# Optimization experiments

Measured on AMD Instinct MI355X. Metric: run time of the kernel, lower is better.

The kernel has to match this reference:

```python
import jax, jax.numpy as jnp
import numpy as np

B, T, C = 32, 256, 512
MAX_LEN = 25


def setup_inputs() -> dict:
    key = jax.random.key(0)
    ks = jax.random.split(key, 6)
    scale = 1.0 / np.sqrt(C)
    return {
        "word_features": jax.random.normal(ks[0], (B, T, C), dtype=jnp.float32),
        "word_fc_w": jax.random.normal(ks[1], (C, C), dtype=jnp.float32) * scale,
        "word_fc_b": jax.random.normal(ks[2], (C,), dtype=jnp.float32) * scale,
        "pos_emb": jax.random.normal(ks[3], (MAX_LEN, C), dtype=jnp.float32),
        "atten_w": jax.random.normal(ks[4], (C,), dtype=jnp.float32) * scale,
        "atten_b": jax.random.normal(ks[5], (1,), dtype=jnp.float32) * scale,
    }


def reference(word_features, word_fc_w, word_fc_b, pos_emb, atten_w, atten_b):
    # word_fc: (b,t,c) -> (b,t,c)
    wf = jnp.einsum("btc,dc->btd", word_features, word_fc_w) + word_fc_b
    # additive (Bahdanau) attention scores over t for each of max_len query positions
    # add_features: (b, L, t, c) = wf[:,None,:,:] + pos_emb[None,:,None,:]
    add_features = jnp.tanh(wf[:, None, :, :] + pos_emb[None, :, None, :])
    # atten_fc: (b, L, t, 1) -> squeeze -> (b, L, t)
    scores = jnp.einsum("bltc,c->blt", add_features, atten_w) + atten_b[0]
    attn = jax.nn.softmax(scores, axis=2)  # softmax over t
    # bmm: (b,L,t) @ (b,t,c) -> (b,L,c)
    pvam_features = jnp.einsum("blt,btc->blc", attn, wf)
    return pvam_features
```

## Files before the change

kernel.cpp:

```cpp
#include <hip/hip_runtime.h>

#define Bn 32
#define Tn 256
#define Cn 512
#define Ln 25

typedef _Float16 h8 __attribute__((ext_vector_type(8)));
typedef _Float16 h8v __attribute__((ext_vector_type(8)));
typedef __attribute__((ext_vector_type(4))) float f32x4;

#define SCALE2LOG2E 2.885390081777927f

#if __has_builtin(__builtin_amdgcn_exp2f)
#define EXP2(x) __builtin_amdgcn_exp2f(x)
#else
#define EXP2(x) __expf(0.69314718056f * (x))
#endif

#define DPP_ADD(v, ctrl) \
    ((v) + __int_as_float(__builtin_amdgcn_update_dpp(0, __float_as_int(v), ctrl, 0xf, 0xf, true)))

#define NA_OCT (Bn * Tn * Cn / 8)
#define NW_OCT (Cn * Cn / 8)
__global__ __launch_bounds__(256) void k_convert(
        const float* __restrict__ A, const float* __restrict__ W,
        _Float16* __restrict__ A2, _Float16* __restrict__ W2) {
    int idx = blockIdx.x * 256 + threadIdx.x;
    const float* src;
    _Float16* dst;
    int off;
    if (idx < NA_OCT) { src = A; dst = A2; off = idx * 8; }
    else              { src = W; dst = W2; off = (idx - NA_OCT) * 8; }
    float4 v0 = *(const float4*)&src[off];
    float4 v1 = *(const float4*)&src[off + 4];
    h8v o;
    o[0] = (_Float16)v0.x; o[1] = (_Float16)v0.y;
    o[2] = (_Float16)v0.z; o[3] = (_Float16)v0.w;
    o[4] = (_Float16)v1.x; o[5] = (_Float16)v1.y;
    o[6] = (_Float16)v1.z; o[7] = (_Float16)v1.w;
    *(h8v*)&dst[off] = o;
}

#define BM 128
#define BN 64
#define BKg 64
__global__ __launch_bounds__(256) void k_gemm(
        const _Float16* __restrict__ A2, const _Float16* __restrict__ W2,
        const float* __restrict__ bias, float* __restrict__ wf) {
    __shared__ _Float16 As[BM * BKg];
    __shared__ _Float16 Ws[BN * BKg];
    const int tid  = threadIdx.x;
    const int lane = tid & 63;
    const int wv   = tid >> 6;
    const int m0 = blockIdx.y * BM;
    const int n0 = blockIdx.x * BN;
    const int wm = (wv >> 1) * 64;
    const int wn = (wv & 1) * 32;
    const int r = lane & 15, q = lane >> 4;

    const _Float16* gA[4];
    const _Float16* gW[2];
    #pragma unroll
    for (int rr = 0; rr < 4; ++rr) {
        int p = rr * 256 + tid;
        int row = p >> 3, pk = p & 7;
        int lk = pk ^ (row & 7);
        gA[rr] = A2 + (size_t)(m0 + row) * Cn + lk * 8;
    }
    #pragma unroll
    for (int rr = 0; rr < 2; ++rr) {
        int p = rr * 256 + tid;
        int row = p >> 3, pk = p & 7;
        int lk = pk ^ (row & 7);
        gW[rr] = W2 + (size_t)(n0 + row) * Cn + lk * 8;
    }

    f32x4 acc[4][2];
    #pragma unroll
    for (int mi = 0; mi < 4; ++mi)
        #pragma unroll
        for (int ni = 0; ni < 2; ++ni) acc[mi][ni] = (f32x4){0.f, 0.f, 0.f, 0.f};

    for (int kt = 0; kt < Cn / BKg; ++kt) {
        __syncthreads();
        #pragma unroll
        for (int rr = 0; rr < 4; ++rr) {
            __builtin_amdgcn_global_load_lds(
                (const __attribute__((address_space(1))) unsigned int*)gA[rr],
                (__attribute__((address_space(3))) unsigned int*)(As + (rr * 256 + wv * 64) * 8),
                16, 0, 0);
            gA[rr] += BKg;
        }
        #pragma unroll
        for (int rr = 0; rr < 2; ++rr) {
            __builtin_amdgcn_global_load_lds(
                (const __attribute__((address_space(1))) unsigned int*)gW[rr],
                (__attribute__((address_space(3))) unsigned int*)(Ws + (rr * 256 + wv * 64) * 8),
                16, 0, 0);
            gW[rr] += BKg;
        }
        __syncthreads();

        h8 af[4][2], bfr[2][2];
        #pragma unroll
        for (int mi = 0; mi < 4; ++mi)
            #pragma unroll
            for (int kk = 0; kk < 2; ++kk) {
                int row = wm + mi * 16 + r;
                int phys = (kk * 4 + q) ^ (r & 7);
                af[mi][kk] = *(const h8*)&As[row * BKg + phys * 8];
            }
        #pragma unroll
        for (int ni = 0; ni < 2; ++ni)
            #pragma unroll
            for (int kk = 0; kk < 2; ++kk) {
                int row = wn + ni * 16 + r;
                int phys = (kk * 4 + q) ^ (r & 7);
                bfr[ni][kk] = *(const h8*)&Ws[row * BKg + phys * 8];
            }
        #pragma unroll
        for (int kk = 0; kk < 2; ++kk)
            #pragma unroll
            for (int mi = 0; mi < 4; ++mi)
                #pragma unroll
                for (int ni = 0; ni < 2; ++ni)
                    acc[mi][ni] = __builtin_amdgcn_mfma_f32_16x16x32_f16(
                        af[mi][kk], bfr[ni][kk], acc[mi][ni], 0, 0, 0);
    }

    #pragma unroll
    for (int ni = 0; ni < 2; ++ni) {
        const float bv = bias[n0 + wn + ni * 16 + r];
        #pragma unroll
        for (int mi = 0; mi < 4; ++mi)
            #pragma unroll
            for (int reg = 0; reg < 4; ++reg) {
                int row = m0 + wm + mi * 16 + q * 4 + reg;
                int col = n0 + wn + ni * 16 + r;
                wf[(size_t)row * Cn + col] = acc[mi][ni][reg] + bv;
            }
    }
}

__global__ __launch_bounds__(512) void k_scores(
        const float* __restrict__ wf, const float* __restrict__ pos,
        const float* __restrict__ aw, float* __restrict__ scores) {
    __shared__ float part[4 * Ln * 8];
    const int tid  = threadIdx.x;
    const int lane = tid & 63;
    const int wv   = tid >> 6;
    const int tl   = wv >> 1;
    const int ch   = wv & 1;
    const int t    = blockIdx.x * 4 + tl;
    const int b    = blockIdx.y;
    const int co   = ch * 256 + lane * 4;

    float4 w = *(const float4*)&wf[(b * Tn + t) * Cn + co];
    w.x *= SCALE2LOG2E; w.y *= SCALE2LOG2E; w.z *= SCALE2LOG2E; w.w *= SCALE2LOG2E;
    const float4 a = *(const float4*)&aw[co];
    const float U = (a.x + a.y) + (a.z + a.w);
    float4 u;
    u.x = -2.f * a.x; u.y = -2.f * a.y; u.z = -2.f * a.z; u.w = -2.f * a.w;

    const float* pp = pos + co;
    float* prt = &part[tl * Ln * 8 + ch * 4 + (lane >> 4)];
    const bool writer = ((lane & 15) == 0);

    #pragma unroll
    for (int lo = 0; lo < 5; ++lo) {
        float4 pv[5];
        #pragma unroll
        for (int j = 0; j < 5; ++j)
            pv[j] = *(const float4*)(pp + (lo * 5 + j) * Cn);
        #pragma unroll
        for (int j = 0; j < 5; ++j) {
            const float4 p = pv[j];
            float s = U;
            s = fmaf(u.x, __builtin_amdgcn_rcpf(1.f + EXP2(fmaf(SCALE2LOG2E, p.x, w.x))), s);
            s = fmaf(u.y, __builtin_amdgcn_rcpf(1.f + EXP2(fmaf(SCALE2LOG2E, p.y, w.y))), s);
            s = fmaf(u.z, __builtin_amdgcn_rcpf(1.f + EXP2(fmaf(SCALE2LOG2E, p.z, w.z))), s);
            s = fmaf(u.w, __builtin_amdgcn_rcpf(1.f + EXP2(fmaf(SCALE2LOG2E, p.w, w.w))), s);
            s = DPP_ADD(s, 0xB1);
            s = DPP_ADD(s, 0x4E);
            s = DPP_ADD(s, 0x141);
            s = DPP_ADD(s, 0x140);
            if (writer) prt[(lo * 5 + j) * 8] = s;
        }
    }
    __syncthreads();
    if (tid < 4 * Ln) {
        int tl2 = tid / Ln, l2 = tid - tl2 * Ln;
        const float* q = &part[(tl2 * Ln + l2) * 8];
        float v = ((q[0] + q[1]) + (q[2] + q[3])) + ((q[4] + q[5]) + (q[6] + q[7]));
        scores[(b * Ln + l2) * Tn + blockIdx.x * 4 + tl2] = v;
    }
}

__global__ __launch_bounds__(512) void k_pvam(
        const float* __restrict__ wf, const float* __restrict__ scores,
        float* __restrict__ out) {
    __shared__ float buf[8 * Ln * 64];
    __shared__ float pT[Tn][28];
    const int tid = threadIdx.x;
    const int cx  = blockIdx.x;
    const int b   = blockIdx.y;

    const float* sc = scores + b * Ln * Tn;
    for (int i = tid * 4; i < Ln * Tn; i += 2048)
        *(float4*)&buf[i] = *(const float4*)&sc[i];
    __syncthreads();

    const int lane = tid & 63;
    const int wv   = tid >> 6;

    for (int l = wv; l < Ln; l += 8) {
        float v0 = buf[l * Tn + lane];
        float v1 = buf[l * Tn + 64 + lane];
        float v2 = buf[l * Tn + 128 + lane];
        float v3 = buf[l * Tn + 192 + lane];
        float m = fmaxf(fmaxf(v0, v1), fmaxf(v2, v3));
        #pragma unroll
        for (int o = 32; o > 0; o >>= 1) m = fmaxf(m, __shfl_xor(m, o));
        float e0 = __expf(v0 - m), e1 = __expf(v1 - m);
        float e2 = __expf(v2 - m), e3 = __expf(v3 - m);
        float s = e0 + e1 + e2 + e3;
        #pragma unroll
        for (int o = 32; o > 0; o >>= 1) s += __shfl_xor(s, o);
        float rs = __builtin_amdgcn_rcpf(s);
        pT[lane][l]       = e0 * rs;
        pT[64 + lane][l]  = e1 * rs;
        pT[128 + lane][l] = e2 * rs;
        pT[192 + lane][l] = e3 * rs;
    }
    __syncthreads();

    const int c = cx * 64 + lane;
    float acc[Ln];
    #pragma unroll
    for (int l = 0; l < Ln; ++l) acc[l] = 0.f;

    const float* wfp = wf + (b * Tn + wv * 32) * Cn + c;
    for (int tt = 0; tt < 32; ++tt) {
        float w = wfp[tt * Cn];
        const float* pp = &pT[wv * 32 + tt][0];
        float p[Ln];
        *(float4*)&p[0]  = *(const float4*)&pp[0];
        *(float4*)&p[4]  = *(const float4*)&pp[4];
        *(float4*)&p[8]  = *(const float4*)&pp[8];
        *(float4*)&p[12] = *(const float4*)&pp[12];
        *(float4*)&p[16] = *(const float4*)&pp[16];
        *(float4*)&p[20] = *(const float4*)&pp[20];
        p[24] = pp[24];
        #pragma unroll
        for (int l = 0; l < Ln; ++l) acc[l] = fmaf(p[l], w, acc[l]);
    }

    __syncthreads();
    #pragma unroll
    for (int l = 0; l < Ln; ++l)
        buf[(wv * Ln + l) * 64 + lane] = acc[l];
    __syncthreads();
    for (int idx = tid; idx < Ln * 64; idx += 512) {
        int l = idx >> 6, cc = idx & 63;
        float v = 0.f;
        #pragma unroll
        for (int w = 0; w < 8; ++w) v += buf[(w * Ln + l) * 64 + cc];
        out[(b * Ln + l) * Cn + cx * 64 + cc] = v;
    }
}

extern "C" void kernel_launch(void* const* d_in, const int* in_sizes, int n_in,
                              void* d_out, int out_size, void* d_ws, size_t ws_size,
                              hipStream_t stream) {
    const float* A    = (const float*)d_in[0];
    const float* W    = (const float*)d_in[1];
    const float* bias = (const float*)d_in[2];
    const float* pos  = (const float*)d_in[3];
    const float* aw   = (const float*)d_in[4];

    char* ws = (char*)d_ws;
    float*     wf     = (float*)ws;
    float*     scores = (float*)(ws + 16777216ull);
    _Float16*  A2     = (_Float16*)(ws + 20054016ull);
    _Float16*  W2     = (_Float16*)(ws + 28442624ull);
    float* out = (float*)d_out;

    k_convert<<<(NA_OCT + NW_OCT) / 256, 256, 0, stream>>>(A, W, A2, W2);
    k_gemm<<<dim3(Cn / BN, (Bn * Tn) / BM), 256, 0, stream>>>(A2, W2, bias, wf);
    k_scores<<<dim3(Tn / 4, Bn), 512, 0, stream>>>(wf, pos, aw, scores);
    k_pvam<<<dim3(Cn / 64, Bn), 512, 0, stream>>>(wf, scores, out);
}
```

Baseline: 121.6 us.

## Fuse all four stages into one cooperative persistent kernel with grid syncs

Replaces the convert, GEMM, scores and pvam launches with a single cooperative kernel of 256 blocks that runs each phase in a grid-stride loop, separated by grid.sync(). The softmax probabilities now go to a global buffer P, and the pvam phase reads them from there. The goal is to remove per-launch overhead and the gaps between kernels. In exchange, each phase is limited to 256 blocks. The GEMM uses smaller per-wave tiles, only 32 blocks do the softmax, and every grid barrier adds its own cost.

```diff
diff --git a/kernel.cpp b/kernel.cpp
--- a/kernel.cpp
+++ b/kernel.cpp
@@ -1,4 +1,7 @@
 #include <hip/hip_runtime.h>
+#include <hip/hip_cooperative_groups.h>
+
+namespace cg = cooperative_groups;
 
 #define Bn 32
 #define Tn 256
@@ -6,7 +9,6 @@
 #define Ln 25
 
 typedef _Float16 h8 __attribute__((ext_vector_type(8)));
-typedef _Float16 h8v __attribute__((ext_vector_type(8)));
 typedef __attribute__((ext_vector_type(4))) float f32x4;
 
 #define SCALE2LOG2E 2.885390081777927f
@@ -22,250 +24,236 @@
 
 #define NA_OCT (Bn * Tn * Cn / 8)
 #define NW_OCT (Cn * Cn / 8)
-__global__ __launch_bounds__(256) void k_convert(
+
+__global__ __launch_bounds__(512, 2) void k_mega(
         const float* __restrict__ A, const float* __restrict__ W,
-        _Float16* __restrict__ A2, _Float16* __restrict__ W2) {
-    int idx = blockIdx.x * 256 + threadIdx.x;
-    const float* src;
-    _Float16* dst;
-    int off;
-    if (idx < NA_OCT) { src = A; dst = A2; off = idx * 8; }
-    else              { src = W; dst = W2; off = (idx - NA_OCT) * 8; }
-    float4 v0 = *(const float4*)&src[off];
-    float4 v1 = *(const float4*)&src[off + 4];
-    h8v o;
-    o[0] = (_Float16)v0.x; o[1] = (_Float16)v0.y;
-    o[2] = (_Float16)v0.z; o[3] = (_Float16)v0.w;
-    o[4] = (_Float16)v1.x; o[5] = (_Float16)v1.y;
-    o[6] = (_Float16)v1.z; o[7] = (_Float16)v1.w;
-    *(h8v*)&dst[off] = o;
-}
-
-#define BM 128
-#define BN 64
-#define BKg 64
-__global__ __launch_bounds__(256) void k_gemm(
-        const _Float16* __restrict__ A2, const _Float16* __restrict__ W2,
-        const float* __restrict__ bias, float* __restrict__ wf) {
-    __shared__ _Float16 As[BM * BKg];
-    __shared__ _Float16 Ws[BN * BKg];
+        const float* __restrict__ bias, const float* __restrict__ pos,
+        const float* __restrict__ aw,
+        float* __restrict__ wf, float* __restrict__ scores, float* __restrict__ P,
+        _Float16* __restrict__ A2, _Float16* __restrict__ W2,
+        float* __restrict__ out) {
+    __shared__ union {
+        struct { _Float16 As[128 * 64]; _Float16 Ws[64 * 64]; } g;
+        float part[4 * Ln * 8];
+        float sm[Ln * Tn];
+        float red[8 * Ln * 64];
+    } su;
+    cg::grid_group grid = cg::this_grid();
     const int tid  = threadIdx.x;
     const int lane = tid & 63;
     const int wv   = tid >> 6;
-    const int m0 = blockIdx.y * BM;
-    const int n0 = blockIdx.x * BN;
-    const int wm = (wv >> 1) * 64;
-    const int wn = (wv & 1) * 32;
-    const int r = lane & 15, q = lane >> 4;
-
-    const _Float16* gA[4];
-    const _Float16* gW[2];
-    #pragma unroll
-    for (int rr = 0; rr < 4; ++rr) {
-        int p = rr * 256 + tid;
-        int row = p >> 3, pk = p & 7;
-        int lk = pk ^ (row & 7);
-        gA[rr] = A2 + (size_t)(m0 + row) * Cn + lk * 8;
-    }
-    #pragma unroll
-    for (int rr = 0; rr < 2; ++rr) {
-        int p = rr * 256 + tid;
-        int row = p >> 3, pk = p & 7;
-        int lk = pk ^ (row & 7);
-        gW[rr] = W2 + (size_t)(n0 + row) * Cn + lk * 8;
-    }
-
-    f32x4 acc[4][2];
-    #pragma unroll
-    for (int mi = 0; mi < 4; ++mi)
+    const int bid  = blockIdx.x;
+
+    for (int idx = bid * 512 + tid; idx < NA_OCT + NW_OCT; idx += 256 * 512) {
+        const float* src; _Float16* dst; int off;
+        if (idx < NA_OCT) { src = A; dst = A2; off = idx * 8; }
+        else              { src = W; dst = W2; off = (idx - NA_OCT) * 8; }
+        float4 v0 = *(const float4*)&src[off];
+        float4 v1 = *(const float4*)&src[off + 4];
+        h8 o;
+        o[0] = (_Float16)v0.x; o[1] = (_Float16)v0.y;
+        o[2] = (_Float16)v0.z; o[3] = (_Float16)v0.w;
+        o[4] = (_Float16)v1.x; o[5] = (_Float16)v1.y;
+        o[6] = (_Float16)v1.z; o[7] = (_Float16)v1.w;
+        *(h8*)&dst[off] = o;
+    }
+    grid.sync();
+
+    {
+        const int wm = (wv >> 1) * 32;
+        const int wn = (wv & 1) * 32;
+        const int r = lane & 15, q = lane >> 4;
+        for (int tile = bid; tile < 512; tile += 256) {
+            const int m0 = (tile >> 3) * 128;
+            const int n0 = (tile & 7) * 64;
+            f32x4 acc[2][2];
+            #pragma unroll
+            for (int mi = 0; mi < 2; ++mi)
+                #pragma unroll
+                for (int ni = 0; ni < 2; ++ni) acc[mi][ni] = (f32x4){0.f, 0.f, 0.f, 0.f};
+
+            for (int kt = 0; kt < 8; ++kt) {
+                __syncthreads();
+                #pragma unroll
+                for (int rr = 0; rr < 2; ++rr) {
+                    int p = rr * 512 + tid;
+                    int row = p >> 3, pk = p & 7;
+                    int lk = pk ^ (row & 7);
+                    __builtin_amdgcn_global_load_lds(
+                        (const __attribute__((address_space(1))) unsigned int*)
+                            (A2 + (size_t)(m0 + row) * Cn + kt * 64 + lk * 8),
+                        (__attribute__((address_space(3))) unsigned int*)
+                            (su.g.As + (rr * 512 + wv * 64) * 8),
+                        16, 0, 0);
+                }
+                {
+                    int p = tid;
+                    int row = p >> 3, pk = p & 7;
+                    int lk = pk ^ (row & 7);
+                    __builtin_amdgcn_global_load_lds(
+                        (const __attribute__((address_space(1))) unsigned int*)
+                            (W2 + (size_t)(n0 + row) * Cn + kt * 64 + lk * 8),
+                        (__attribute__((address_space(3))) unsigned int*)
+                            (su.g.Ws + (wv * 64) * 8),
+                        16, 0, 0);
+                }
+                __syncthreads();
+
+                h8 af[2][2], bfr[2][2];
+                #pragma unroll
+                for (int mi = 0; mi < 2; ++mi)
+                    #pragma unroll
+                    for (int kk = 0; kk < 2; ++kk) {
+                        int row = wm + mi * 16 + r;
+                        int phys = (kk * 4 + q) ^ (r & 7);
+                        af[mi][kk] = *(const h8*)&su.g.As[row * 64 + phys * 8];
+                    }
+                #pragma unroll
+                for (int ni = 0; ni < 2; ++ni)
+                    #pragma unroll
+                    for (int kk = 0; kk < 2; ++kk) {
+                        int row = wn + ni * 16 + r;
+                        int phys = (kk * 4 + q) ^ (r & 7);
+                        bfr[ni][kk] = *(const h8*)&su.g.Ws[row * 64 + phys * 8];
+                    }
+                #pragma unroll
+                for (int kk = 0; kk < 2; ++kk)
+                    #pragma unroll
+                    for (int mi = 0; mi < 2; ++mi)
+                        #pragma unroll
+                        for (int ni = 0; ni < 2; ++ni)
+                            acc[mi][ni] = __builtin_amdgcn_mfma_f32_16x16x32_f16(
+                                af[mi][kk], bfr[ni][kk], acc[mi][ni], 0, 0, 0);
+            }
+
+            #pragma unroll
+            for (int ni = 0; ni < 2; ++ni) {
+                const float bv = bias[n0 + wn + ni * 16 + r];
+                #pragma unroll
+                for (int mi = 0; mi < 2; ++mi)
+                    #pragma unroll
+                    for (int reg = 0; reg < 4; ++reg) {
+                        int row = m0 + wm + mi * 16 + q * 4 + reg;
+                        int col = n0 + wn + ni * 16 + r;
+                        wf[(size_t)row * Cn + col] = acc[mi][ni][reg] + bv;
+                    }
+            }
+            __syncthreads();
+        }
+    }
+    grid.sync();
+
+    {
+        const int tl = wv >> 1;
+        const int ch = wv & 1;
+        const int co = ch * 256 + lane * 4;
+        const float4 a = *(const float4*)&aw[co];
+        const float U = (a.x + a.y) + (a.z + a.w);
+        float4 u;
+        u.x = -2.f * a.x; u.y = -2.f * a.y; u.z = -2.f * a.z; u.w = -2.f * a.w;
+        const float* pp = pos + co;
+        float* prt = &su.part[tl * Ln * 8 + ch * 4 + (lane >> 4)];
+        const bool writer = ((lane & 15) == 0);
+
+        for (int wk = bid; wk < 2048; wk += 256) {
+            const int tx = wk & 63, b = wk >> 6;
+            const int t = tx * 4 + tl;
+            float4 w = *(const float4*)&wf[(size_t)(b * Tn + t) * Cn + co];
+            w.x *= SCALE2LOG2E; w.y *= SCALE2LOG2E; w.z *= SCALE2LOG2E; w.w *= SCALE2LOG2E;
+
+            #pragma unroll
+            for (int lo = 0; lo < 5; ++lo) {
+                float4 pv[5];
+                #pragma unroll
+                for (int j = 0; j < 5; ++j)
+                    pv[j] = *(const float4*)(pp + (lo * 5 + j) * Cn);
+                #pragma unroll
+                for (int j = 0; j < 5; ++j) {
+                    const float4 p = pv[j];
+                    float s = U;
+                    s = fmaf(u.x, __builtin_amdgcn_rcpf(1.f + EXP2(fmaf(SCALE2LOG2E, p.x, w.x))), s);
+                    s = fmaf(u.y, __builtin_amdgcn_rcpf(1.f + EXP2(fmaf(SCALE2LOG2E, p.y, w.y))), s);
+                    s = fmaf(u.z, __builtin_amdgcn_rcpf(1.f + EXP2(fmaf(SCALE2LOG2E, p.z, w.z))), s);
+                    s = fmaf(u.w, __builtin_amdgcn_rcpf(1.f + EXP2(fmaf(SCALE2LOG2E, p.w, w.w))), s);
+                    s = DPP_ADD(s, 0xB1);
+                    s = DPP_ADD(s, 0x4E);
+                    s = DPP_ADD(s, 0x141);
+                    s = DPP_ADD(s, 0x140);
+                    if (writer) prt[(lo * 5 + j) * 8] = s;
+                }
+            }
+            __syncthreads();
+            if (tid < 4 * Ln) {
+                int tl2 = tid / Ln, l2 = tid - tl2 * Ln;
+                const float* q2 = &su.part[(tl2 * Ln + l2) * 8];
+                float v = ((q2[0] + q2[1]) + (q2[2] + q2[3])) + ((q2[4] + q2[5]) + (q2[6] + q2[7]));
+                scores[(size_t)(b * Ln + l2) * Tn + tx * 4 + tl2] = v;
+            }
+            __syncthreads();
+        }
+    }
+    grid.sync();
+
+    if (bid < Bn) {
+        const int b = bid;
+        const float* sc = scores + (size_t)b * Ln * Tn;
+        for (int i = tid * 4; i < Ln * Tn; i += 2048)
+            *(float4*)&su.sm[i] = *(const float4*)&sc[i];
+        __syncthreads();
+        for (int l = wv; l < Ln; l += 8) {
+            float v0 = su.sm[l * Tn + lane];
+            float v1 = su.sm[l * Tn + 64 + lane];
+            float v2 = su.sm[l * Tn + 128 + lane];
+            float v3 = su.sm[l * Tn + 192 + lane];
+            float m = fmaxf(fmaxf(v0, v1), fmaxf(v2, v3));
+            #pragma unroll
+            for (int o = 32; o > 0; o >>= 1) m = fmaxf(m, __shfl_xor(m, o));
+            float e0 = __expf(v0 - m), e1 = __expf(v1 - m);
+            float e2 = __expf(v2 - m), e3 = __expf(v3 - m);
+            float s = e0 + e1 + e2 + e3;
+            #pragma unroll
+            for (int o = 32; o > 0; o >>= 1) s += __shfl_xor(s, o);
+            float rs = __builtin_amdgcn_rcpf(s);
+            float* pr = P + ((size_t)(b * Tn) + lane) * 32 + l;
+            pr[0]        = e0 * rs;
+            pr[64 * 32]  = e1 * rs;
+            pr[128 * 32] = e2 * rs;
+            pr[192 * 32] = e3 * rs;
+        }
+    }
+    grid.sync();
+
+    {
+        const int cx = bid & 7, b = bid >> 3;
+        const int c = cx * 64 + lane;
+        float acc[Ln];
         #pragma unroll
-        for (int ni = 0; ni < 2; ++ni) acc[mi][ni] = (f32x4){0.f, 0.f, 0.f, 0.f};
-
-    for (int kt = 0; kt < Cn / BKg; ++kt) {
+        for (int l = 0; l < Ln; ++l) acc[l] = 0.f;
+
+        const float* wfp = wf + ((size_t)(b * Tn + wv * 32)) * Cn + c;
+        const float* pb  = P + ((size_t)(b * Tn + wv * 32)) * 32;
+        for (int tt = 0; tt < 32; ++tt) {
+            float w = wfp[tt * Cn];
+            float p[28];
+            #pragma unroll
+            for (int j = 0; j < 7; ++j)
+                *(float4*)&p[j * 4] = *(const float4*)(pb + tt * 32 + j * 4);
+            #pragma unroll
+            for (int l = 0; l < Ln; ++l) acc[l] = fmaf(p[l], w, acc[l]);
+        }
+
         __syncthreads();
         #pragma unroll
-        for (int rr = 0; rr < 4; ++rr) {
-            __builtin_amdgcn_global_load_lds(
-                (const __attribute__((address_space(1))) unsigned int*)gA[rr],
-                (__attribute__((address_space(3))) unsigned int*)(As + (rr * 256 + wv * 64) * 8),
-                16, 0, 0);
-            gA[rr] += BKg;
-        }
-        #pragma unroll
-        for (int rr = 0; rr < 2; ++rr) {
-            __builtin_amdgcn_global_load_lds(
-                (const __attribute__((address_space(1))) unsigned int*)gW[rr],
-                (__attribute__((address_space(3))) unsigned int*)(Ws + (rr * 256 + wv * 64) * 8),
-                16, 0, 0);
-            gW[rr] += BKg;
-        }
+        for (int l = 0; l < Ln; ++l)
+            su.red[(wv * Ln + l) * 64 + lane] = acc[l];
         __syncthreads();
-
-        h8 af[4][2], bfr[2][2];
-        #pragma unroll
-        for (int mi = 0; mi < 4; ++mi)
-            #pragma unroll
-            for (int kk = 0; kk < 2; ++kk) {
-                int row = wm + mi * 16 + r;
-                int phys = (kk * 4 + q) ^ (r & 7);
-                af[mi][kk] = *(const h8*)&As[row * BKg + phys * 8];
-            }
-        #pragma unroll
-        for (int ni = 0; ni < 2; ++ni)
-            #pragma unroll
-            for (int kk = 0; kk < 2; ++kk) {
-                int row = wn + ni * 16 + r;
-                int phys = (kk * 4 + q) ^ (r & 7);
-                bfr[ni][kk] = *(const h8*)&Ws[row * BKg + phys * 8];
-            }
-        #pragma unroll
-        for (int kk = 0; kk < 2; ++kk)
-            #pragma unroll
-            for (int mi = 0; mi < 4; ++mi)
-                #pragma unroll
-                for (int ni = 0; ni < 2; ++ni)
-                    acc[mi][ni] = __builtin_amdgcn_mfma_f32_16x16x32_f16(
-                        af[mi][kk], bfr[ni][kk], acc[mi][ni], 0, 0, 0);
-    }
-
-    #pragma unroll
-    for (int ni = 0; ni < 2; ++ni) {
-        const float bv = bias[n0 + wn + ni * 16 + r];
-        #pragma unroll
-        for (int mi = 0; mi < 4; ++mi)
-            #pragma unroll
-            for (int reg = 0; reg < 4; ++reg) {
-                int row = m0 + wm + mi * 16 + q * 4 + reg;
-                int col = n0 + wn + ni * 16 + r;
-                wf[(size_t)row * Cn + col] = acc[mi][ni][reg] + bv;
-            }
-    }
-}
-
-__global__ __launch_bounds__(512) void k_scores(
-        const float* __restrict__ wf, const float* __restrict__ pos,
-        const float* __restrict__ aw, float* __restrict__ scores) {
-    __shared__ float part[4 * Ln * 8];
-    const int tid  = threadIdx.x;
-    const int lane = tid & 63;
-    const int wv   = tid >> 6;
-    const int tl   = wv >> 1;
-    const int ch   = wv & 1;
-    const int t    = blockIdx.x * 4 + tl;
-    const int b    = blockIdx.y;
-    const int co   = ch * 256 + lane * 4;
-
-    float4 w = *(const float4*)&wf[(b * Tn + t) * Cn + co];
-    w.x *= SCALE2LOG2E; w.y *= SCALE2LOG2E; w.z *= SCALE2LOG2E; w.w *= SCALE2LOG2E;
-    const float4 a = *(const float4*)&aw[co];
-    const float U = (a.x + a.y) + (a.z + a.w);
-    float4 u;
-    u.x = -2.f * a.x; u.y = -2.f * a.y; u.z = -2.f * a.z; u.w = -2.f * a.w;
-
-    const float* pp = pos + co;
-    float* prt = &part[tl * Ln * 8 + ch * 4 + (lane >> 4)];
-    const bool writer = ((lane & 15) == 0);
-
-    #pragma unroll
-    for (int lo = 0; lo < 5; ++lo) {
-        float4 pv[5];
-        #pragma unroll
-        for (int j = 0; j < 5; ++j)
-            pv[j] = *(const float4*)(pp + (lo * 5 + j) * Cn);
-        #pragma unroll
-        for (int j = 0; j < 5; ++j) {
-            const float4 p = pv[j];
-            float s = U;
-            s = fmaf(u.x, __builtin_amdgcn_rcpf(1.f + EXP2(fmaf(SCALE2LOG2E, p.x, w.x))), s);
-            s = fmaf(u.y, __builtin_amdgcn_rcpf(1.f + EXP2(fmaf(SCALE2LOG2E, p.y, w.y))), s);
-            s = fmaf(u.z, __builtin_amdgcn_rcpf(1.f + EXP2(fmaf(SCALE2LOG2E, p.z, w.z))), s);
-            s = fmaf(u.w, __builtin_amdgcn_rcpf(1.f + EXP2(fmaf(SCALE2LOG2E, p.w, w.w))), s);
-            s = DPP_ADD(s, 0xB1);
-            s = DPP_ADD(s, 0x4E);
-            s = DPP_ADD(s, 0x141);
-            s = DPP_ADD(s, 0x140);
-            if (writer) prt[(lo * 5 + j) * 8] = s;
-        }
-    }
-    __syncthreads();
-    if (tid < 4 * Ln) {
-        int tl2 = tid / Ln, l2 = tid - tl2 * Ln;
-        const float* q = &part[(tl2 * Ln + l2) * 8];
-        float v = ((q[0] + q[1]) + (q[2] + q[3])) + ((q[4] + q[5]) + (q[6] + q[7]));
-        scores[(b * Ln + l2) * Tn + blockIdx.x * 4 + tl2] = v;
-    }
-}
-
-__global__ __launch_bounds__(512) void k_pvam(
-        const float* __restrict__ wf, const float* __restrict__ scores,
-        float* __restrict__ out) {
-    __shared__ float buf[8 * Ln * 64];
-    __shared__ float pT[Tn][28];
-    const int tid = threadIdx.x;
-    const int cx  = blockIdx.x;
-    const int b   = blockIdx.y;
-
-    const float* sc = scores + b * Ln * Tn;
-    for (int i = tid * 4; i < Ln * Tn; i += 2048)
-        *(float4*)&buf[i] = *(const float4*)&sc[i];
-    __syncthreads();
-
-    const int lane = tid & 63;
-    const int wv   = tid >> 6;
-
-    for (int l = wv; l < Ln; l += 8) {
-        float v0 = buf[l * Tn + lane];
-        float v1 = buf[l * Tn + 64 + lane];
-        float v2 = buf[l * Tn + 128 + lane];
-        float v3 = buf[l * Tn + 192 + lane];
-        float m = fmaxf(fmaxf(v0, v1), fmaxf(v2, v3));
-        #pragma unroll
-        for (int o = 32; o > 0; o >>= 1) m = fmaxf(m, __shfl_xor(m, o));
-        float e0 = __expf(v0 - m), e1 = __expf(v1 - m);
-        float e2 = __expf(v2 - m), e3 = __expf(v3 - m);
-        float s = e0 + e1 + e2 + e3;
-        #pragma unroll
-        for (int o = 32; o > 0; o >>= 1) s += __shfl_xor(s, o);
-        float rs = __builtin_amdgcn_rcpf(s);
-        pT[lane][l]       = e0 * rs;
-        pT[64 + lane][l]  = e1 * rs;
-        pT[128 + lane][l] = e2 * rs;
-        pT[192 + lane][l] = e3 * rs;
-    }
-    __syncthreads();
-
-    const int c = cx * 64 + lane;
-    float acc[Ln];
-    #pragma unroll
-    for (int l = 0; l < Ln; ++l) acc[l] = 0.f;
-
-    const float* wfp = wf + (b * Tn + wv * 32) * Cn + c;
-    for (int tt = 0; tt < 32; ++tt) {
-        float w = wfp[tt * Cn];
-        const float* pp = &pT[wv * 32 + tt][0];
-        float p[Ln];
-        *(float4*)&p[0]  = *(const float4*)&pp[0];
-        *(float4*)&p[4]  = *(const float4*)&pp[4];
-        *(float4*)&p[8]  = *(const float4*)&pp[8];
-        *(float4*)&p[12] = *(const float4*)&pp[12];
-        *(float4*)&p[16] = *(const float4*)&pp[16];
-        *(float4*)&p[20] = *(const float4*)&pp[20];
-        p[24] = pp[24];
-        #pragma unroll
-        for (int l = 0; l < Ln; ++l) acc[l] = fmaf(p[l], w, acc[l]);
-    }
-
-    __syncthreads();
-    #pragma unroll
-    for (int l = 0; l < Ln; ++l)
-        buf[(wv * Ln + l) * 64 + lane] = acc[l];
-    __syncthreads();
-    for (int idx = tid; idx < Ln * 64; idx += 512) {
-        int l = idx >> 6, cc = idx & 63;
-        float v = 0.f;
-        #pragma unroll
-        for (int w = 0; w < 8; ++w) v += buf[(w * Ln + l) * 64 + cc];
-        out[(b * Ln + l) * Cn + cx * 64 + cc] = v;
+        for (int i = tid; i < Ln * 64; i += 512) {
+            int l = i >> 6, cc = i & 63;
+            float v = 0.f;
+            #pragma unroll
+            for (int w8 = 0; w8 < 8; ++w8) v += su.red[(w8 * Ln + l) * 64 + cc];
+            out[((size_t)b * Ln + l) * Cn + cx * 64 + cc] = v;
+        }
     }
 }
 
@@ -281,12 +269,13 @@
     char* ws = (char*)d_ws;
     float*     wf     = (float*)ws;
     float*     scores = (float*)(ws + 16777216ull);
-    _Float16*  A2     = (_Float16*)(ws + 20054016ull);
-    _Float16*  W2     = (_Float16*)(ws + 28442624ull);
-    float* out = (float*)d_out;
-
-    k_convert<<<(NA_OCT + NW_OCT) / 256, 256, 0, stream>>>(A, W, A2, W2);
-    k_gemm<<<dim3(Cn / BN, (Bn * Tn) / BM), 256, 0, stream>>>(A2, W2, bias, wf);
-    k_scores<<<dim3(Tn / 4, Bn), 512, 0, stream>>>(wf, pos, aw, scores);
-    k_pvam<<<dim3(Cn / 64, Bn), 512, 0, stream>>>(wf, scores, out);
+    float*     P      = (float*)(ws + 17596416ull);
+    _Float16*  A2     = (_Float16*)(ws + 18644992ull);
+    _Float16*  W2     = (_Float16*)(ws + 27033600ull);
+    float* outp = (float*)d_out;
+
+    void* args[] = { (void*)&A, (void*)&W, (void*)&bias, (void*)&pos, (void*)&aw,
+                     (void*)&wf, (void*)&scores, (void*)&P, (void*)&A2, (void*)&W2,
+                     (void*)&outp };
+    hipLaunchCooperativeKernel((const void*)k_mega, dim3(256), dim3(512), args, 0, stream);
 }
```

Result: slower. 286.3 us (+135.4%).

## Fuse fp32-to-fp16 conversion into GEMM operand loading and enlarge tiles

Applied to the files above, without the earlier changes.

Removes the separate conversion kernel. The GEMM now reads fp32 A and W directly, converts them to fp16 in registers, and stores them into padded LDS tiles. The tile grows to 128x128 with 512 threads, BK=32, and a register prefetch of the next k-slice. This saves one launch and the fp16 intermediate round trip through global memory. In exchange it gives up the async global_load_lds path, reads twice as many bytes per element, and needs more barriers per k-step.

```diff
diff --git a/kernel.cpp b/kernel.cpp
--- a/kernel.cpp
+++ b/kernel.cpp
@@ -6,7 +6,6 @@
 #define Ln 25
 
 typedef _Float16 h8 __attribute__((ext_vector_type(8)));
-typedef _Float16 h8v __attribute__((ext_vector_type(8)));
 typedef __attribute__((ext_vector_type(4))) float f32x4;
 
 #define SCALE2LOG2E 2.885390081777927f
@@ -20,60 +19,30 @@
 #define DPP_ADD(v, ctrl) \
     ((v) + __int_as_float(__builtin_amdgcn_update_dpp(0, __float_as_int(v), ctrl, 0xf, 0xf, true)))
 
-#define NA_OCT (Bn * Tn * Cn / 8)
-#define NW_OCT (Cn * Cn / 8)
-__global__ __launch_bounds__(256) void k_convert(
+#define BM 128
+#define BN 128
+#define BKh 32
+#define LDST 40
+__global__ __launch_bounds__(512, 4) void k_gemm(
         const float* __restrict__ A, const float* __restrict__ W,
-        _Float16* __restrict__ A2, _Float16* __restrict__ W2) {
-    int idx = blockIdx.x * 256 + threadIdx.x;
-    const float* src;
-    _Float16* dst;
-    int off;
-    if (idx < NA_OCT) { src = A; dst = A2; off = idx * 8; }
-    else              { src = W; dst = W2; off = (idx - NA_OCT) * 8; }
-    float4 v0 = *(const float4*)&src[off];
-    float4 v1 = *(const float4*)&src[off + 4];
-    h8v o;
-    o[0] = (_Float16)v0.x; o[1] = (_Float16)v0.y;
-    o[2] = (_Float16)v0.z; o[3] = (_Float16)v0.w;
-    o[4] = (_Float16)v1.x; o[5] = (_Float16)v1.y;
-    o[6] = (_Float16)v1.z; o[7] = (_Float16)v1.w;
-    *(h8v*)&dst[off] = o;
-}
-
-#define BM 128
-#define BN 64
-#define BKg 64
-__global__ __launch_bounds__(256) void k_gemm(
-        const _Float16* __restrict__ A2, const _Float16* __restrict__ W2,
         const float* __restrict__ bias, float* __restrict__ wf) {
-    __shared__ _Float16 As[BM * BKg];
-    __shared__ _Float16 Ws[BN * BKg];
+    __shared__ _Float16 As[BM * LDST];
+    __shared__ _Float16 Ws[BN * LDST];
     const int tid  = threadIdx.x;
     const int lane = tid & 63;
     const int wv   = tid >> 6;
+    const int n0 = blockIdx.x * BN;
     const int m0 = blockIdx.y * BM;
-    const int n0 = blockIdx.x * BN;
-    const int wm = (wv >> 1) * 64;
-    const int wn = (wv & 1) * 32;
+    const int wm = (wv & 1) * 64;
+    const int wn = (wv >> 1) * 32;
     const int r = lane & 15, q = lane >> 4;
 
-    const _Float16* gA[4];
-    const _Float16* gW[2];
-    #pragma unroll
-    for (int rr = 0; rr < 4; ++rr) {
-        int p = rr * 256 + tid;
-        int row = p >> 3, pk = p & 7;
-        int lk = pk ^ (row & 7);
-        gA[rr] = A2 + (size_t)(m0 + row) * Cn + lk * 8;
-    }
-    #pragma unroll
-    for (int rr = 0; rr < 2; ++rr) {
-        int p = rr * 256 + tid;
-        int row = p >> 3, pk = p & 7;
-        int lk = pk ^ (row & 7);
-        gW[rr] = W2 + (size_t)(n0 + row) * Cn + lk * 8;
-    }
+    const int srow = tid >> 2;
+    const int skc  = tid & 3;
+    const float* gA = A + (size_t)(m0 + srow) * Cn + skc * 8;
+    const float* gW = W + (size_t)(n0 + srow) * Cn + skc * 8;
+    _Float16* lA = &As[srow * LDST + skc * 8];
+    _Float16* lW = &Ws[srow * LDST + skc * 8];
 
     f32x4 acc[4][2];
     #pragma unroll
@@ -81,51 +50,46 @@
         #pragma unroll
         for (int ni = 0; ni < 2; ++ni) acc[mi][ni] = (f32x4){0.f, 0.f, 0.f, 0.f};
 
-    for (int kt = 0; kt < Cn / BKg; ++kt) {
+    float4 ra0 = *(const float4*)gA;
+    float4 ra1 = *(const float4*)(gA + 4);
+    float4 rw0 = *(const float4*)gW;
+    float4 rw1 = *(const float4*)(gW + 4);
+
+    for (int kt = 0; kt < Cn / BKh; ++kt) {
+        if (kt > 0) __syncthreads();
+        h8 ha, hw;
+        ha[0] = (_Float16)ra0.x; ha[1] = (_Float16)ra0.y;
+        ha[2] = (_Float16)ra0.z; ha[3] = (_Float16)ra0.w;
+        ha[4] = (_Float16)ra1.x; ha[5] = (_Float16)ra1.y;
+        ha[6] = (_Float16)ra1.z; ha[7] = (_Float16)ra1.w;
+        hw[0] = (_Float16)rw0.x; hw[1] = (_Float16)rw0.y;
+        hw[2] = (_Float16)rw0.z; hw[3] = (_Float16)rw0.w;
+        hw[4] = (_Float16)rw1.x; hw[5] = (_Float16)rw1.y;
+        hw[6] = (_Float16)rw1.z; hw[7] = (_Float16)rw1.w;
+        *(h8*)lA = ha;
+        *(h8*)lW = hw;
         __syncthreads();
-        #pragma unroll
-        for (int rr = 0; rr < 4; ++rr) {
-            __builtin_amdgcn_global_load_lds(
-                (const __attribute__((address_space(1))) unsigned int*)gA[rr],
-                (__attribute__((address_space(3))) unsigned int*)(As + (rr * 256 + wv * 64) * 8),
-                16, 0, 0);
-            gA[rr] += BKg;
+        if (kt < Cn / BKh - 1) {
+            gA += BKh; gW += BKh;
+            ra0 = *(const float4*)gA;
+            ra1 = *(const float4*)(gA + 4);
+            rw0 = *(const float4*)gW;
+            rw1 = *(const float4*)(gW + 4);
         }
-        #pragma unroll
-        for (int rr = 0; rr < 2; ++rr) {
-            __builtin_amdgcn_global_load_lds(
-                (const __attribute__((address_space(1))) unsigned int*)gW[rr],
-                (__attribute__((address_space(3))) unsigned int*)(Ws + (rr * 256 + wv * 64) * 8),
-                16, 0, 0);
-            gW[rr] += BKg;
-        }
-        __syncthreads();
-
-        h8 af[4][2], bfr[2][2];
+
+        h8 af[4], bf[2];
+        #pragma unroll
+        for (int mi = 0; mi < 4; ++mi)
+            af[mi] = *(const h8*)&As[(wm + mi * 16 + r) * LDST + q * 8];
+        #pragma unroll
+        for (int ni = 0; ni < 2; ++ni)
+            bf[ni] = *(const h8*)&Ws[(wn + ni * 16 + r) * LDST + q * 8];
         #pragma unroll
         for (int mi = 0; mi < 4; ++mi)
             #pragma unroll
-            for (int kk = 0; kk < 2; ++kk) {
-                int row = wm + mi * 16 + r;
-                int phys = (kk * 4 + q) ^ (r & 7);
-                af[mi][kk] = *(const h8*)&As[row * BKg + phys * 8];
-            }
-        #pragma unroll
-        for (int ni = 0; ni < 2; ++ni)
-            #pragma unroll
-            for (int kk = 0; kk < 2; ++kk) {
-                int row = wn + ni * 16 + r;
-                int phys = (kk * 4 + q) ^ (r & 7);
-                bfr[ni][kk] = *(const h8*)&Ws[row * BKg + phys * 8];
-            }
-        #pragma unroll
-        for (int kk = 0; kk < 2; ++kk)
-            #pragma unroll
-            for (int mi = 0; mi < 4; ++mi)
-                #pragma unroll
-                for (int ni = 0; ni < 2; ++ni)
-                    acc[mi][ni] = __builtin_amdgcn_mfma_f32_16x16x32_f16(
-                        af[mi][kk], bfr[ni][kk], acc[mi][ni], 0, 0, 0);
+            for (int ni = 0; ni < 2; ++ni)
+                acc[mi][ni] = __builtin_amdgcn_mfma_f32_16x16x32_f16(
+                    af[mi], bf[ni], acc[mi][ni], 0, 0, 0);
     }
 
     #pragma unroll
@@ -279,14 +243,11 @@
     const float* aw   = (const float*)d_in[4];
 
     char* ws = (char*)d_ws;
-    float*     wf     = (float*)ws;
-    float*     scores = (float*)(ws + 16777216ull);
-    _Float16*  A2     = (_Float16*)(ws + 20054016ull);
-    _Float16*  W2     = (_Float16*)(ws + 28442624ull);
+    float* wf     = (float*)ws;
+    float* scores = (float*)(ws + 16777216ull);
     float* out = (float*)d_out;
 
-    k_convert<<<(NA_OCT + NW_OCT) / 256, 256, 0, stream>>>(A, W, A2, W2);
-    k_gemm<<<dim3(Cn / BN, (Bn * Tn) / BM), 256, 0, stream>>>(A2, W2, bias, wf);
+    k_gemm<<<dim3(Cn / BN, (Bn * Tn) / BM), 512, 0, stream>>>(A, W, bias, wf);
     k_scores<<<dim3(Tn / 4, Bn), 512, 0, stream>>>(wf, pos, aw, scores);
     k_pvam<<<dim3(Cn / 64, Bn), 512, 0, stream>>>(wf, scores, out);
 }
```

Measured after the change: 123.2 us. About the same (+1.3%).

## Fuse attention-score computation into GEMM epilogue with per-column-tile partial scores

Applied to the files above, without the earlier changes.

Removes the separate scores kernel. The tanh-attention partial dot products are now computed directly from the GEMM accumulators in registers, over each block's 64-channel slice. Each block writes partial scores to one of 8 column-tile planes, and the pvam kernel sums the 8 planes when it loads the scores. This avoids re-reading wf from memory and saves one launch. In exchange the GEMM epilogue gets longer, LDS use grows through the union, and the pvam prologue reads 8x more score data.

```diff
diff --git a/kernel.cpp b/kernel.cpp
--- a/kernel.cpp
+++ b/kernel.cpp
@@ -6,7 +6,6 @@
 #define Ln 25
 
 typedef _Float16 h8 __attribute__((ext_vector_type(8)));
-typedef _Float16 h8v __attribute__((ext_vector_type(8)));
 typedef __attribute__((ext_vector_type(4))) float f32x4;
 
 #define SCALE2LOG2E 2.885390081777927f
@@ -33,12 +32,12 @@
     else              { src = W; dst = W2; off = (idx - NA_OCT) * 8; }
     float4 v0 = *(const float4*)&src[off];
     float4 v1 = *(const float4*)&src[off + 4];
-    h8v o;
+    h8 o;
     o[0] = (_Float16)v0.x; o[1] = (_Float16)v0.y;
     o[2] = (_Float16)v0.z; o[3] = (_Float16)v0.w;
     o[4] = (_Float16)v1.x; o[5] = (_Float16)v1.y;
     o[6] = (_Float16)v1.z; o[7] = (_Float16)v1.w;
-    *(h8v*)&dst[off] = o;
+    *(h8*)&dst[off] = o;
 }
 
 #define BM 128
@@ -46,14 +45,18 @@
 #define BKg 64
 __global__ __launch_bounds__(256) void k_gemm(
         const _Float16* __restrict__ A2, const _Float16* __restrict__ W2,
-        const float* __restrict__ bias, float* __restrict__ wf) {
-    __shared__ _Float16 As[BM * BKg];
-    __shared__ _Float16 Ws[BN * BKg];
+        const float* __restrict__ bias, float* __restrict__ wf,
+        const float* __restrict__ pos, const float* __restrict__ aw,
+        float* __restrict__ sc8) {
+    __shared__ union {
+        struct { _Float16 As[BM * BKg]; _Float16 Ws[BN * BKg]; } g;
+        struct { float scp[2 * BM * Ln]; float posl[Ln * BN]; } e;
+    } su;
     const int tid  = threadIdx.x;
     const int lane = tid & 63;
     const int wv   = tid >> 6;
+    const int n0 = blockIdx.x * BN;
     const int m0 = blockIdx.y * BM;
-    const int n0 = blockIdx.x * BN;
     const int wm = (wv >> 1) * 64;
     const int wn = (wv & 1) * 32;
     const int r = lane & 15, q = lane >> 4;
@@ -87,7 +90,7 @@
         for (int rr = 0; rr < 4; ++rr) {
             __builtin_amdgcn_global_load_lds(
                 (const __attribute__((address_space(1))) unsigned int*)gA[rr],
-                (__attribute__((address_space(3))) unsigned int*)(As + (rr * 256 + wv * 64) * 8),
+                (__attribute__((address_space(3))) unsigned int*)(su.g.As + (rr * 256 + wv * 64) * 8),
                 16, 0, 0);
             gA[rr] += BKg;
         }
@@ -95,7 +98,7 @@
         for (int rr = 0; rr < 2; ++rr) {
             __builtin_amdgcn_global_load_lds(
                 (const __attribute__((address_space(1))) unsigned int*)gW[rr],
-                (__attribute__((address_space(3))) unsigned int*)(Ws + (rr * 256 + wv * 64) * 8),
+                (__attribute__((address_space(3))) unsigned int*)(su.g.Ws + (rr * 256 + wv * 64) * 8),
                 16, 0, 0);
             gW[rr] += BKg;
         }
@@ -108,7 +111,7 @@
             for (int kk = 0; kk < 2; ++kk) {
                 int row = wm + mi * 16 + r;
                 int phys = (kk * 4 + q) ^ (r & 7);
-                af[mi][kk] = *(const h8*)&As[row * BKg + phys * 8];
+                af[mi][kk] = *(const h8*)&su.g.As[row * BKg + phys * 8];
             }
         #pragma unroll
         for (int ni = 0; ni < 2; ++ni)
@@ -116,7 +119,7 @@
             for (int kk = 0; kk < 2; ++kk) {
                 int row = wn + ni * 16 + r;
                 int phys = (kk * 4 + q) ^ (r & 7);
-                bfr[ni][kk] = *(const h8*)&Ws[row * BKg + phys * 8];
+                bfr[ni][kk] = *(const h8*)&su.g.Ws[row * BKg + phys * 8];
             }
         #pragma unroll
         for (int kk = 0; kk < 2; ++kk)
@@ -137,67 +140,58 @@
             for (int reg = 0; reg < 4; ++reg) {
                 int row = m0 + wm + mi * 16 + q * 4 + reg;
                 int col = n0 + wn + ni * 16 + r;
-                wf[(size_t)row * Cn + col] = acc[mi][ni][reg] + bv;
-            }
-    }
-}
-
-__global__ __launch_bounds__(512) void k_scores(
-        const float* __restrict__ wf, const float* __restrict__ pos,
-        const float* __restrict__ aw, float* __restrict__ scores) {
-    __shared__ float part[4 * Ln * 8];
-    const int tid  = threadIdx.x;
-    const int lane = tid & 63;
-    const int wv   = tid >> 6;
-    const int tl   = wv >> 1;
-    const int ch   = wv & 1;
-    const int t    = blockIdx.x * 4 + tl;
-    const int b    = blockIdx.y;
-    const int co   = ch * 256 + lane * 4;
-
-    float4 w = *(const float4*)&wf[(b * Tn + t) * Cn + co];
-    w.x *= SCALE2LOG2E; w.y *= SCALE2LOG2E; w.z *= SCALE2LOG2E; w.w *= SCALE2LOG2E;
-    const float4 a = *(const float4*)&aw[co];
-    const float U = (a.x + a.y) + (a.z + a.w);
-    float4 u;
-    u.x = -2.f * a.x; u.y = -2.f * a.y; u.z = -2.f * a.z; u.w = -2.f * a.w;
-
-    const float* pp = pos + co;
-    float* prt = &part[tl * Ln * 8 + ch * 4 + (lane >> 4)];
-    const bool writer = ((lane & 15) == 0);
-
-    #pragma unroll
-    for (int lo = 0; lo < 5; ++lo) {
-        float4 pv[5];
-        #pragma unroll
-        for (int j = 0; j < 5; ++j)
-            pv[j] = *(const float4*)(pp + (lo * 5 + j) * Cn);
-        #pragma unroll
-        for (int j = 0; j < 5; ++j) {
-            const float4 p = pv[j];
-            float s = U;
-            s = fmaf(u.x, __builtin_amdgcn_rcpf(1.f + EXP2(fmaf(SCALE2LOG2E, p.x, w.x))), s);
-            s = fmaf(u.y, __builtin_amdgcn_rcpf(1.f + EXP2(fmaf(SCALE2LOG2E, p.y, w.y))), s);
-            s = fmaf(u.z, __builtin_amdgcn_rcpf(1.f + EXP2(fmaf(SCALE2LOG2E, p.z, w.z))), s);
-            s = fmaf(u.w, __builtin_amdgcn_rcpf(1.f + EXP2(fmaf(SCALE2LOG2E, p.w, w.w))), s);
-            s = DPP_ADD(s, 0xB1);
-            s = DPP_ADD(s, 0x4E);
-            s = DPP_ADD(s, 0x141);
-            s = DPP_ADD(s, 0x140);
-            if (writer) prt[(lo * 5 + j) * 8] = s;
-        }
-    }
-    __syncthreads();
-    if (tid < 4 * Ln) {
-        int tl2 = tid / Ln, l2 = tid - tl2 * Ln;
-        const float* q = &part[(tl2 * Ln + l2) * 8];
-        float v = ((q[0] + q[1]) + (q[2] + q[3])) + ((q[4] + q[5]) + (q[6] + q[7]));
-        scores[(b * Ln + l2) * Tn + blockIdx.x * 4 + tl2] = v;
+                float v = acc[mi][ni][reg] + bv;
+                wf[(size_t)row * Cn + col] = v;
+                acc[mi][ni][reg] = SCALE2LOG2E * v;
+            }
+    }
+
+    __syncthreads();
+    for (int i = tid; i < Ln * BN; i += 256) {
+        int l = i >> 6, c = i & 63;
+        su.e.posl[i] = pos[l * Cn + n0 + c];
+    }
+    const float aw0 = aw[n0 + wn + r];
+    const float aw1 = aw[n0 + wn + 16 + r];
+    const float u0 = -2.f * aw0, u1 = -2.f * aw1;
+    const float Ul = aw0 + aw1;
+    const int wnb = wv & 1;
+    __syncthreads();
+
+    for (int l = 0; l < Ln; ++l) {
+        const float p0 = su.e.posl[l * BN + wn + r];
+        const float p1 = su.e.posl[l * BN + wn + 16 + r];
+        #pragma unroll
+        for (int mi = 0; mi < 4; ++mi)
+            #pragma unroll
+            for (int reg = 0; reg < 4; ++reg) {
+                float s = Ul;
+                s = fmaf(u0, __builtin_amdgcn_rcpf(
+                        1.f + EXP2(fmaf(SCALE2LOG2E, p0, acc[mi][0][reg]))), s);
+                s = fmaf(u1, __builtin_amdgcn_rcpf(
+                        1.f + EXP2(fmaf(SCALE2LOG2E, p1, acc[mi][1][reg]))), s);
+                s = DPP_ADD(s, 0xB1);
+                s = DPP_ADD(s, 0x4E);
+                s = DPP_ADD(s, 0x141);
+                s = DPP_ADD(s, 0x140);
+                if (r == mi * 4 + reg)
+                    su.e.scp[(wnb * BM + wm + mi * 16 + q * 4 + reg) * Ln + l] = s;
+            }
+    }
+    __syncthreads();
+
+    const int b  = blockIdx.y >> 1;
+    const int t0 = (blockIdx.y & 1) * BM;
+    float* plane = sc8 + ((size_t)blockIdx.x * Bn + b) * (Ln * Tn);
+    for (int i = tid; i < BM * Ln; i += 256) {
+        int l = i >> 7, row = i & 127;
+        float v = su.e.scp[row * Ln + l] + su.e.scp[(BM + row) * Ln + l];
+        plane[l * Tn + t0 + row] = v;
     }
 }
 
 __global__ __launch_bounds__(512) void k_pvam(
-        const float* __restrict__ wf, const float* __restrict__ scores,
+        const float* __restrict__ wf, const float* __restrict__ sc8,
         float* __restrict__ out) {
     __shared__ float buf[8 * Ln * 64];
     __shared__ float pT[Tn][28];
@@ -205,9 +199,17 @@
     const int cx  = blockIdx.x;
     const int b   = blockIdx.y;
 
-    const float* sc = scores + b * Ln * Tn;
-    for (int i = tid * 4; i < Ln * Tn; i += 2048)
-        *(float4*)&buf[i] = *(const float4*)&sc[i];
+    const size_t PL = (size_t)Bn * Ln * Tn;
+    const float* sc = sc8 + (size_t)b * (Ln * Tn);
+    for (int i = tid * 4; i < Ln * Tn; i += 2048) {
+        float4 v = *(const float4*)&sc[i];
+        #pragma unroll
+        for (int p = 1; p < 8; ++p) {
+            float4 s = *(const float4*)&sc[p * PL + i];
+            v.x += s.x; v.y += s.y; v.z += s.z; v.w += s.w;
+        }
+        *(float4*)&buf[i] = v;
+    }
     __syncthreads();
 
     const int lane = tid & 63;
@@ -279,14 +281,13 @@
     const float* aw   = (const float*)d_in[4];
 
     char* ws = (char*)d_ws;
-    float*     wf     = (float*)ws;
-    float*     scores = (float*)(ws + 16777216ull);
-    _Float16*  A2     = (_Float16*)(ws + 20054016ull);
-    _Float16*  W2     = (_Float16*)(ws + 28442624ull);
+    float*     wf  = (float*)ws;
+    float*     sc8 = (float*)(ws + 16777216ull);
+    _Float16*  A2  = (_Float16*)(ws + 23330816ull);
+    _Float16*  W2  = (_Float16*)(ws + 31719424ull);
     float* out = (float*)d_out;
 
     k_convert<<<(NA_OCT + NW_OCT) / 256, 256, 0, stream>>>(A, W, A2, W2);
-    k_gemm<<<dim3(Cn / BN, (Bn * Tn) / BM), 256, 0, stream>>>(A2, W2, bias, wf);
-    k_scores<<<dim3(Tn / 4, Bn), 512, 0, stream>>>(wf, pos, aw, scores);
-    k_pvam<<<dim3(Cn / 64, Bn), 512, 0, stream>>>(wf, scores, out);
-}
+    k_gemm<<<dim3(Cn / BN, (Bn * Tn) / BM), 256, 0, stream>>>(A2, W2, bias, wf, pos, aw, sc8);
+    k_pvam<<<dim3(Cn / 64, Bn), 512, 0, stream>>>(wf, sc8, out);
+}
```

Result: slower. 141.5 us (+16.3%).
